# Performance work log

Hardware: AMD Instinct MI355X
Metric: run time of the kernel (lower is better)

Reference implementation:

```python
import jax, jax.numpy as jnp
import numpy as np

BN_EPS = 1e-5


def setup_inputs() -> dict:
    key = jax.random.key(0)
    ks = jax.random.split(key, 8)
    B, S, D, H, O = 4, 25000, 128, 128, 128
    N, E = B * S, 600000
    x = jax.random.normal(ks[0], (B, S, D), dtype=jnp.float32)
    edge_index = jax.random.randint(ks[1], (2, E), 0, N)
    W1 = jax.random.normal(ks[2], (D, H), dtype=jnp.float32) * (1.0 / np.sqrt(D))
    b1 = jnp.zeros((H,), jnp.float32)
    gamma1 = jnp.ones((H,), jnp.float32)
    beta1 = jnp.zeros((H,), jnp.float32)
    W2 = jax.random.normal(ks[3], (H, O), dtype=jnp.float32) * (1.0 / np.sqrt(H))
    b2 = jnp.zeros((O,), jnp.float32)
    return {"x": x, "edge_index": edge_index, "W1": W1, "b1": b1,
            "gamma1": gamma1, "beta1": beta1, "W2": W2, "b2": b2}


def _gcn_norm(edge_index, num_nodes, dtype):
    # PyG gcn_norm: add self-loops, symmetric D^-1/2 (A+I) D^-1/2 edge weights.
    row, col = edge_index
    loop = jnp.arange(num_nodes, dtype=row.dtype)
    row_f = jnp.concatenate([row, loop])
    col_f = jnp.concatenate([col, loop])
    deg = jax.ops.segment_sum(jnp.ones(row_f.shape, dtype), row_f,
                              num_segments=num_nodes)
    dis = jnp.where(deg > 0, jax.lax.rsqrt(jnp.maximum(deg, 1e-12)), 0.0)
    norm = dis[row_f] * dis[col_f]  # [E + N]
    return row_f, col_f, norm


def _gcn_conv(h, W, b, row_f, col_f, norm, num_nodes):
    hw = h @ W                       # [N, out]
    msg = hw[col_f] * norm[:, None]  # gather + scale, [E+N, out]
    out = jax.ops.segment_sum(msg, row_f, num_segments=num_nodes)
    return out + b


def reference(x, edge_index, W1, b1, gamma1, beta1, W2, b2):
    B, S, D = x.shape
    N = B * S
    h = x.reshape(N, D)
    row_f, col_f, norm = _gcn_norm(edge_index, N, h.dtype)
    # layer 1: GCNConv -> BatchNorm (batch stats) -> ReLU (dropout inactive in eval)
    h = _gcn_conv(h, W1, b1, row_f, col_f, norm, N)
    mean = jnp.mean(h, axis=0)
    var = jnp.mean(jnp.square(h - mean), axis=0)
    h = gamma1 * (h - mean) * jax.lax.rsqrt(var + BN_EPS) + beta1
    h = jax.nn.relu(h)
    # layer 2: final GCNConv
    h = _gcn_conv(h, W2, b2, row_f, col_f, norm, N)
    return h.reshape(B, S, -1)
```

## Files before the change

### kernel.cpp

```cpp
#include <hip/hip_runtime.h>

#define DIM 128
#define BN_EPS 1e-5f
#define STAT_COPIES 64

typedef short short8 __attribute__((ext_vector_type(8)));
typedef float floatx4 __attribute__((ext_vector_type(4)));

__device__ __forceinline__ unsigned short f2bf(float f) {
    unsigned int u = __builtin_bit_cast(unsigned int, f);
    u += 0x7FFFu + ((u >> 16) & 1u);
    return (unsigned short)(u >> 16);
}
__device__ __forceinline__ float bf2f(unsigned short h) {
    return __builtin_bit_cast(float, (unsigned int)h << 16);
}


__global__ __launch_bounds__(256) void deg_convw_kernel(
    const int* __restrict__ row, int* __restrict__ deg, int* __restrict__ rank,
    int E, int degB,
    const float* __restrict__ W1, const float* __restrict__ W2,
    unsigned short* __restrict__ wfrag)
{
    if ((int)blockIdx.x < degB) {
        int e = blockIdx.x * 256 + threadIdx.x;
        if (e < E) rank[e] = atomicAdd(&deg[row[e]], 1);
    } else {
        int s = (blockIdx.x - degB) * 256 + threadIdx.x;
        if (s >= 4096) return;
        int m  = s >> 11;
        int s2 = s & 2047;
        int kt = s2 >> 9;
        int nt = (s2 >> 6) & 7;
        int l  = s2 & 63;
        const float* W = m ? W2 : W1;
        unsigned short* o = wfrag + (size_t)m * 16384 + (size_t)s2 * 8;
        int k0 = kt * 32 + (l >> 4) * 8;
        int n0 = nt * 16 + (l & 15);
        #pragma unroll
        for (int j = 0; j < 8; ++j) o[j] = f2bf(W[(k0 + j) * DIM + n0]);
    }
}


__global__ __launch_bounds__(256) void scan_block_kernel(const int* __restrict__ deg,
                                                         int* __restrict__ rowptr,
                                                         int* __restrict__ aux,
                                                         float* __restrict__ dis, int n) {
    __shared__ int ls[256];
    const int base = blockIdx.x * 1024;
    const int t = threadIdx.x;
    int v[4]; int s = 0;
    #pragma unroll
    for (int k = 0; k < 4; ++k) {
        int i = base + t * 4 + k;
        v[k] = (i < n) ? deg[i] : 0;
        s += v[k];
    }
    ls[t] = s;
    __syncthreads();
    for (int off = 1; off < 256; off <<= 1) {
        int x = (t >= off) ? ls[t - off] : 0;
        __syncthreads();
        ls[t] += x;
        __syncthreads();
    }
    int excl = ls[t] - s;
    if (t == 255) aux[blockIdx.x] = ls[255];
    #pragma unroll
    for (int k = 0; k < 4; ++k) {
        int i = base + t * 4 + k;
        if (i < n) {
            rowptr[i] = excl;
            dis[i] = rsqrtf((float)(v[k] + 1));
        }
        excl += v[k];
    }
}


__global__ __launch_bounds__(256) void add_offsets_kernel(
    const int* __restrict__ rowptr, const int* __restrict__ deg,
    const int* __restrict__ aux, int2* __restrict__ rp2, int n)
{
    __shared__ int red[256];
    const int t = threadIdx.x;
    red[t] = (t < (int)blockIdx.x) ? aux[t] : 0;
    __syncthreads();
    for (int off = 128; off > 0; off >>= 1) {
        if (t < off) red[t] += red[t + off];
        __syncthreads();
    }
    const int base = red[0];
    #pragma unroll
    for (int k = 0; k < 4; ++k) {
        int i = blockIdx.x * 1024 + t * 4 + k;
        if (i < n) {
            int st = rowptr[i] + base;
            rp2[i] = make_int2(st, st + deg[i]);
        }
    }
}


__global__ __launch_bounds__(256) void scatter_gemm1_kernel(
    const int* __restrict__ row, const int* __restrict__ col,
    const int* __restrict__ rank, const float* __restrict__ dis,
    const int2* __restrict__ rp2, int2* __restrict__ epack, int E, int scatS,
    const float* __restrict__ A, const unsigned short* __restrict__ wfrag,
    unsigned short* __restrict__ C, int n, int gemmG)
{
    const int grp = blockIdx.x / 5;
    const int off = blockIdx.x % 5;
    if (off < 3) {
        const int sId = grp * 3 + off;
        if (sId >= scatS) return;
        int e = sId * 256 + threadIdx.x;
        if (e >= E) return;
        int r = row[e], c = col[e];
        int pos = rp2[r].x + rank[e];
        float nrm = dis[r] * dis[c];
        epack[pos] = make_int2(c, __builtin_bit_cast(int, nrm));
    } else {
        const int gId = grp * 2 + (off - 3);
        if (gId >= gemmG) return;
        const int tid  = threadIdx.x;
        const int row0 = gId * 64;
        const int wave = tid >> 6;
        const int lane = tid & 63;
        const int m    = lane & 15;
        const int quad = lane >> 4;
        const int rowA = row0 + wave * 16 + m;

        short8 af[4];
        if (rowA < n) {
            #pragma unroll
            for (int kt = 0; kt < 4; ++kt) {
                const float* src = A + (size_t)rowA * DIM + kt * 32 + quad * 8;
                float4 v0 = *(const float4*)(src);
                float4 v1 = *(const float4*)(src + 4);
                af[kt] = (short8){ (short)f2bf(v0.x), (short)f2bf(v0.y),
                                   (short)f2bf(v0.z), (short)f2bf(v0.w),
                                   (short)f2bf(v1.x), (short)f2bf(v1.y),
                                   (short)f2bf(v1.z), (short)f2bf(v1.w) };
            }
        } else {
            #pragma unroll
            for (int kt = 0; kt < 4; ++kt) af[kt] = (short8){0,0,0,0,0,0,0,0};
        }

        floatx4 acc[8];
        #pragma unroll
        for (int nt = 0; nt < 8; ++nt) acc[nt] = (floatx4){0.f, 0.f, 0.f, 0.f};

        #pragma unroll
        for (int nt = 0; nt < 8; ++nt)
            #pragma unroll
            for (int kt = 0; kt < 4; ++kt) {
                short8 bfr = *(const short8*)(wfrag + ((size_t)(kt * 8 + nt) * 64 + lane) * 8);
                acc[nt] = __builtin_amdgcn_mfma_f32_16x16x32_bf16(af[kt], bfr, acc[nt], 0, 0, 0);
            }

        #pragma unroll
        for (int nt = 0; nt < 8; ++nt)
            #pragma unroll
            for (int r = 0; r < 4; ++r) {
                int rr = row0 + wave * 16 + quad * 4 + r;
                if (rr < n) C[(size_t)rr * DIM + nt * 16 + m] = f2bf(acc[nt][r]);
            }
    }
}


__global__ __launch_bounds__(256) void gemm_mfma_bn_kernel(
    const unsigned short* __restrict__ Abf, const unsigned short* __restrict__ wfrag,
    unsigned short* __restrict__ C, int n,
    const float* __restrict__ mi)
{
    const int tid  = threadIdx.x;
    const int row0 = blockIdx.x * 64;
    const int wave = tid >> 6;
    const int lane = tid & 63;
    const int m    = lane & 15;
    const int quad = lane >> 4;
    const int rowA = row0 + wave * 16 + m;

    short8 af[4];
    if (rowA < n) {
        #pragma unroll
        for (int kt = 0; kt < 4; ++kt) {
            const int c0 = kt * 32 + quad * 8;
            short8 v = *(const short8*)(Abf + (size_t)rowA * DIM + c0);
            float4 s0 = *(const float4*)(mi + c0);
            float4 s1 = *(const float4*)(mi + c0 + 4);
            float4 h0 = *(const float4*)(mi + 128 + c0);
            float4 h1 = *(const float4*)(mi + 128 + c0 + 4);
            float f[8];
            #pragma unroll
            for (int j = 0; j < 8; ++j) f[j] = bf2f((unsigned short)v[j]);
            f[0] = fmaxf(fmaf(f[0], s0.x, h0.x), 0.f);
            f[1] = fmaxf(fmaf(f[1], s0.y, h0.y), 0.f);
            f[2] = fmaxf(fmaf(f[2], s0.z, h0.z), 0.f);
            f[3] = fmaxf(fmaf(f[3], s0.w, h0.w), 0.f);
            f[4] = fmaxf(fmaf(f[4], s1.x, h1.x), 0.f);
            f[5] = fmaxf(fmaf(f[5], s1.y, h1.y), 0.f);
            f[6] = fmaxf(fmaf(f[6], s1.z, h1.z), 0.f);
            f[7] = fmaxf(fmaf(f[7], s1.w, h1.w), 0.f);
            af[kt] = (short8){ (short)f2bf(f[0]), (short)f2bf(f[1]),
                               (short)f2bf(f[2]), (short)f2bf(f[3]),
                               (short)f2bf(f[4]), (short)f2bf(f[5]),
                               (short)f2bf(f[6]), (short)f2bf(f[7]) };
        }
    } else {
        #pragma unroll
        for (int kt = 0; kt < 4; ++kt) af[kt] = (short8){0,0,0,0,0,0,0,0};
    }

    floatx4 acc[8];
    #pragma unroll
    for (int nt = 0; nt < 8; ++nt) acc[nt] = (floatx4){0.f, 0.f, 0.f, 0.f};

    #pragma unroll
    for (int nt = 0; nt < 8; ++nt)
        #pragma unroll
        for (int kt = 0; kt < 4; ++kt) {
            short8 bfr = *(const short8*)(wfrag + ((size_t)(kt * 8 + nt) * 64 + lane) * 8);
            acc[nt] = __builtin_amdgcn_mfma_f32_16x16x32_bf16(af[kt], bfr, acc[nt], 0, 0, 0);
        }

    #pragma unroll
    for (int nt = 0; nt < 8; ++nt)
        #pragma unroll
        for (int r = 0; r < 4; ++r) {
            int rr = row0 + wave * 16 + quad * 4 + r;
            if (rr < n) C[(size_t)rr * DIM + nt * 16 + m] = f2bf(acc[nt][r]);
        }
}


__device__ __forceinline__ void acc8(float* acc, uint4 u, float w) {
    unsigned int a[4] = {u.x, u.y, u.z, u.w};
    #pragma unroll
    for (int k = 0; k < 4; ++k) {
        acc[2*k]   = fmaf(bf2f((unsigned short)(a[k] & 0xffff)), w, acc[2*k]);
        acc[2*k+1] = fmaf(bf2f((unsigned short)(a[k] >> 16)),    w, acc[2*k+1]);
    }
}

template <bool OUT_BF16, bool STATS>
__global__ __launch_bounds__(256) void agg_csr_kernel(
    const unsigned short* __restrict__ hw, const float* __restrict__ dis,
    const int2* __restrict__ rp2, const int2* __restrict__ epack,
    const float* __restrict__ bias, void* __restrict__ out_, int n,
    float* __restrict__ stat)
{
    const int sub  = threadIdx.x >> 4;
    const int l    = threadIdx.x & 15;
    const int node = blockIdx.x * 16 + sub;
    const bool valid = node < n;
    const int j = l * 8;

    float acc[8];
    #pragma unroll
    for (int k = 0; k < 8; ++k) acc[k] = 0.f;

    if (valid) {
        const int2 rp = rp2[node];
        {
            const float d = dis[node];
            uint4 u = *(const uint4*)(hw + (size_t)node * DIM + j);
            acc8(acc, u, d * d);
        }

        const int pe = rp.y;
        for (int p = rp.x; p < pe; p += 8) {
            const int pm = pe - 1;
            int2 e[8];
            #pragma unroll
            for (int k = 0; k < 8; ++k) {
                int pk = p + k;
                e[k] = epack[pk < pm ? pk : pm];
            }
            uint4 u[8];
            #pragma unroll
            for (int k = 0; k < 8; ++k)
                u[k] = *(const uint4*)(hw + (size_t)e[k].x * DIM + j);
            #pragma unroll
            for (int k = 0; k < 8; ++k) {
                float w = (p + k < pe) ? __builtin_bit_cast(float, e[k].y) : 0.f;
                acc8(acc, u[k], w);
            }
        }

        float4 b0 = *(const float4*)(bias + j);
        float4 b1 = *(const float4*)(bias + j + 4);
        acc[0] += b0.x; acc[1] += b0.y; acc[2] += b0.z; acc[3] += b0.w;
        acc[4] += b1.x; acc[5] += b1.y; acc[6] += b1.z; acc[7] += b1.w;

        if (OUT_BF16) {
            unsigned short* out = (unsigned short*)out_;
            uint4 o;
            o.x = (unsigned int)f2bf(acc[0]) | ((unsigned int)f2bf(acc[1]) << 16);
            o.y = (unsigned int)f2bf(acc[2]) | ((unsigned int)f2bf(acc[3]) << 16);
            o.z = (unsigned int)f2bf(acc[4]) | ((unsigned int)f2bf(acc[5]) << 16);
            o.w = (unsigned int)f2bf(acc[6]) | ((unsigned int)f2bf(acc[7]) << 16);
            *(uint4*)(out + (size_t)node * DIM + j) = o;
        } else {
            float* out = (float*)out_;
            *(float4*)(out + (size_t)node * DIM + j)     = make_float4(acc[0], acc[1], acc[2], acc[3]);
            *(float4*)(out + (size_t)node * DIM + j + 4) = make_float4(acc[4], acc[5], acc[6], acc[7]);
        }
    }

    if constexpr (STATS) {
        __shared__ float red[16][257];
        #pragma unroll
        for (int k = 0; k < 8; ++k) {
            float a = valid ? acc[k] : 0.f;
            red[sub][j + k]       = a;
            red[sub][128 + j + k] = a * a;
        }
        __syncthreads();
        float t = 0.f;
        #pragma unroll
        for (int r = 0; r < 16; ++r) t += red[r][threadIdx.x];
        atomicAdd(&stat[(blockIdx.x & (STAT_COPIES - 1)) * 256 + threadIdx.x], t);
    }
}


__global__ void bn_finalize_kernel(const float* __restrict__ stat,
                                   const float* __restrict__ gamma,
                                   const float* __restrict__ beta,
                                   float* __restrict__ mi, int n) {
    int c = threadIdx.x;
    if (c < DIM) {
        float s = 0.f, q = 0.f;
        #pragma unroll 4
        for (int cp = 0; cp < STAT_COPIES; ++cp) {
            s += stat[cp * 256 + c];
            q += stat[cp * 256 + 128 + c];
        }
        float mean  = s / (float)n;
        float var   = q / (float)n - mean * mean;
        float istd  = rsqrtf(var + BN_EPS);
        float scale = gamma[c] * istd;
        mi[c]       = scale;
        mi[DIM + c] = fmaf(-mean, scale, beta[c]);
    }
}


extern "C" void kernel_launch(void* const* d_in, const int* in_sizes, int n_in,
                              void* d_out, int out_size, void* d_ws, size_t ws_size,
                              hipStream_t stream)
{
    const float* x      = (const float*)d_in[0];
    const int*   ei     = (const int*)  d_in[1];
    const float* W1     = (const float*)d_in[2];
    const float* b1     = (const float*)d_in[3];
    const float* gamma1 = (const float*)d_in[4];
    const float* beta1  = (const float*)d_in[5];
    const float* W2     = (const float*)d_in[6];
    const float* b2     = (const float*)d_in[7];
    float* out = (float*)d_out;

    const int N = in_sizes[0] / DIM;
    const int E = in_sizes[1] / 2;
    const int* row = ei;
    const int* col = ei + E;

    const int NB    = (N + 1023) / 1024;
    const int degB  = (E + 255) / 256;
    const int gemmB = (N + 63) / 64;
    const int aggB  = (N + 15) / 16;
    const int k4B   = 5 * max((degB + 2) / 3, (gemmB + 1) / 2);

    unsigned short* hw    = (unsigned short*)d_ws;
    unsigned short* h1    = hw + (size_t)N * DIM;
    int2*  epack  = (int2*)(h1 + (size_t)N * DIM);
    int2*  rp2    = epack + E;
    unsigned short* wfrag = (unsigned short*)(rp2 + N);
    float* dis    = (float*)(wfrag + 2 * 16384);
    int*   rank   = (int*)(dis + N);
    int*   rowptr = rank + E;
    int*   aux    = rowptr + N;
    float* mi     = (float*)(aux + 256);
    int*   deg    = (int*)(mi + 256);
    float* stat   = (float*)(deg + N);
    const size_t zero_bytes = (size_t)N * 4 + (size_t)STAT_COPIES * 256 * 4;

    hipMemsetAsync(deg, 0, zero_bytes, stream);

    deg_convw_kernel<<<degB + 16, 256, 0, stream>>>(row, deg, rank, E, degB, W1, W2, wfrag);
    scan_block_kernel<<<NB, 256, 0, stream>>>(deg, rowptr, aux, dis, N);
    add_offsets_kernel<<<NB, 256, 0, stream>>>(rowptr, deg, aux, rp2, N);
    scatter_gemm1_kernel<<<k4B, 256, 0, stream>>>(row, col, rank, dis, rp2, epack, E, degB,
                                                  x, wfrag, hw, N, gemmB);
    agg_csr_kernel<true, true><<<aggB, 256, 0, stream>>>(hw, dis, rp2, epack, b1, h1, N,
                                                         stat);
    bn_finalize_kernel<<<1, DIM, 0, stream>>>(stat, gamma1, beta1, mi, N);
    gemm_mfma_bn_kernel<<<gemmB, 256, 0, stream>>>(h1, wfrag + 16384, hw, N, mi);
    agg_csr_kernel<false, false><<<aggB, 256, 0, stream>>>(hw, dis, rp2, epack, b2, out, N,
                                                           nullptr);
}
```

Before: 261.9 us.

## Reorder layer-2 as aggregate-then-transform and fuse BN/ReLU, aggregation and GEMM

Layer 2 now aggregates the normalized, ReLU'd h1 features first and multiplies by W2 afterwards (A·(h·W) = (A·h)·W). The BN and ReLU are applied on the fly to every gathered neighbor row, and a per-block fp32 FMA GEMM against W2 runs in the same kernel. This removes the separate MFMA GEMM kernel and its bf16 intermediate write and re-read. In exchange BN/ReLU is recomputed once per edge, and the W2 product runs on scalar FMAs reading W2 from global memory instead of using MFMA.

```diff
diff --git a/kernel.cpp b/kernel.cpp
--- a/kernel.cpp
+++ b/kernel.cpp
@@ -20,26 +20,22 @@
 __global__ __launch_bounds__(256) void deg_convw_kernel(
     const int* __restrict__ row, int* __restrict__ deg, int* __restrict__ rank,
     int E, int degB,
-    const float* __restrict__ W1, const float* __restrict__ W2,
-    unsigned short* __restrict__ wfrag)
+    const float* __restrict__ W1, unsigned short* __restrict__ wfrag)
 {
     if ((int)blockIdx.x < degB) {
         int e = blockIdx.x * 256 + threadIdx.x;
         if (e < E) rank[e] = atomicAdd(&deg[row[e]], 1);
     } else {
         int s = (blockIdx.x - degB) * 256 + threadIdx.x;
-        if (s >= 4096) return;
-        int m  = s >> 11;
-        int s2 = s & 2047;
-        int kt = s2 >> 9;
-        int nt = (s2 >> 6) & 7;
-        int l  = s2 & 63;
-        const float* W = m ? W2 : W1;
-        unsigned short* o = wfrag + (size_t)m * 16384 + (size_t)s2 * 8;
+        if (s >= 2048) return;
+        int kt = s >> 9;
+        int nt = (s >> 6) & 7;
+        int l  = s & 63;
+        unsigned short* o = wfrag + (size_t)s * 8;
         int k0 = kt * 32 + (l >> 4) * 8;
         int n0 = nt * 16 + (l & 15);
         #pragma unroll
-        for (int j = 0; j < 8; ++j) o[j] = f2bf(W[(k0 + j) * DIM + n0]);
+        for (int j = 0; j < 8; ++j) o[j] = f2bf(W1[(k0 + j) * DIM + n0]);
     }
 }
 
@@ -173,72 +169,6 @@
 }
 
 
-__global__ __launch_bounds__(256) void gemm_mfma_bn_kernel(
-    const unsigned short* __restrict__ Abf, const unsigned short* __restrict__ wfrag,
-    unsigned short* __restrict__ C, int n,
-    const float* __restrict__ mi)
-{
-    const int tid  = threadIdx.x;
-    const int row0 = blockIdx.x * 64;
-    const int wave = tid >> 6;
-    const int lane = tid & 63;
-    const int m    = lane & 15;
-    const int quad = lane >> 4;
-    const int rowA = row0 + wave * 16 + m;
-
-    short8 af[4];
-    if (rowA < n) {
-        #pragma unroll
-        for (int kt = 0; kt < 4; ++kt) {
-            const int c0 = kt * 32 + quad * 8;
-            short8 v = *(const short8*)(Abf + (size_t)rowA * DIM + c0);
-            float4 s0 = *(const float4*)(mi + c0);
-            float4 s1 = *(const float4*)(mi + c0 + 4);
-            float4 h0 = *(const float4*)(mi + 128 + c0);
-            float4 h1 = *(const float4*)(mi + 128 + c0 + 4);
-            float f[8];
-            #pragma unroll
-            for (int j = 0; j < 8; ++j) f[j] = bf2f((unsigned short)v[j]);
-            f[0] = fmaxf(fmaf(f[0], s0.x, h0.x), 0.f);
-            f[1] = fmaxf(fmaf(f[1], s0.y, h0.y), 0.f);
-            f[2] = fmaxf(fmaf(f[2], s0.z, h0.z), 0.f);
-            f[3] = fmaxf(fmaf(f[3], s0.w, h0.w), 0.f);
-            f[4] = fmaxf(fmaf(f[4], s1.x, h1.x), 0.f);
-            f[5] = fmaxf(fmaf(f[5], s1.y, h1.y), 0.f);
-            f[6] = fmaxf(fmaf(f[6], s1.z, h1.z), 0.f);
-            f[7] = fmaxf(fmaf(f[7], s1.w, h1.w), 0.f);
-            af[kt] = (short8){ (short)f2bf(f[0]), (short)f2bf(f[1]),
-                               (short)f2bf(f[2]), (short)f2bf(f[3]),
-                               (short)f2bf(f[4]), (short)f2bf(f[5]),
-                               (short)f2bf(f[6]), (short)f2bf(f[7]) };
-        }
-    } else {
-        #pragma unroll
-        for (int kt = 0; kt < 4; ++kt) af[kt] = (short8){0,0,0,0,0,0,0,0};
-    }
-
-    floatx4 acc[8];
-    #pragma unroll
-    for (int nt = 0; nt < 8; ++nt) acc[nt] = (floatx4){0.f, 0.f, 0.f, 0.f};
-
-    #pragma unroll
-    for (int nt = 0; nt < 8; ++nt)
-        #pragma unroll
-        for (int kt = 0; kt < 4; ++kt) {
-            short8 bfr = *(const short8*)(wfrag + ((size_t)(kt * 8 + nt) * 64 + lane) * 8);
-            acc[nt] = __builtin_amdgcn_mfma_f32_16x16x32_bf16(af[kt], bfr, acc[nt], 0, 0, 0);
-        }
-
-    #pragma unroll
-    for (int nt = 0; nt < 8; ++nt)
-        #pragma unroll
-        for (int r = 0; r < 4; ++r) {
-            int rr = row0 + wave * 16 + quad * 4 + r;
-            if (rr < n) C[(size_t)rr * DIM + nt * 16 + m] = f2bf(acc[nt][r]);
-        }
-}
-
-
 __device__ __forceinline__ void acc8(float* acc, uint4 u, float w) {
     unsigned int a[4] = {u.x, u.y, u.z, u.w};
     #pragma unroll
@@ -248,11 +178,10 @@
     }
 }
 
-template <bool OUT_BF16, bool STATS>
-__global__ __launch_bounds__(256) void agg_csr_kernel(
+__global__ __launch_bounds__(256) void agg1_kernel(
     const unsigned short* __restrict__ hw, const float* __restrict__ dis,
     const int2* __restrict__ rp2, const int2* __restrict__ epack,
-    const float* __restrict__ bias, void* __restrict__ out_, int n,
+    const float* __restrict__ bias, unsigned short* __restrict__ out, int n,
     float* __restrict__ stat)
 {
     const int sub  = threadIdx.x >> 4;
@@ -298,35 +227,26 @@
         acc[0] += b0.x; acc[1] += b0.y; acc[2] += b0.z; acc[3] += b0.w;
         acc[4] += b1.x; acc[5] += b1.y; acc[6] += b1.z; acc[7] += b1.w;
 
-        if (OUT_BF16) {
-            unsigned short* out = (unsigned short*)out_;
-            uint4 o;
-            o.x = (unsigned int)f2bf(acc[0]) | ((unsigned int)f2bf(acc[1]) << 16);
-            o.y = (unsigned int)f2bf(acc[2]) | ((unsigned int)f2bf(acc[3]) << 16);
-            o.z = (unsigned int)f2bf(acc[4]) | ((unsigned int)f2bf(acc[5]) << 16);
-            o.w = (unsigned int)f2bf(acc[6]) | ((unsigned int)f2bf(acc[7]) << 16);
-            *(uint4*)(out + (size_t)node * DIM + j) = o;
-        } else {
-            float* out = (float*)out_;
-            *(float4*)(out + (size_t)node * DIM + j)     = make_float4(acc[0], acc[1], acc[2], acc[3]);
-            *(float4*)(out + (size_t)node * DIM + j + 4) = make_float4(acc[4], acc[5], acc[6], acc[7]);
-        }
-    }
-
-    if constexpr (STATS) {
-        __shared__ float red[16][257];
-        #pragma unroll
-        for (int k = 0; k < 8; ++k) {
-            float a = valid ? acc[k] : 0.f;
-            red[sub][j + k]       = a;
-            red[sub][128 + j + k] = a * a;
-        }
-        __syncthreads();
-        float t = 0.f;
-        #pragma unroll
-        for (int r = 0; r < 16; ++r) t += red[r][threadIdx.x];
-        atomicAdd(&stat[(blockIdx.x & (STAT_COPIES - 1)) * 256 + threadIdx.x], t);
-    }
+        uint4 o;
+        o.x = (unsigned int)f2bf(acc[0]) | ((unsigned int)f2bf(acc[1]) << 16);
+        o.y = (unsigned int)f2bf(acc[2]) | ((unsigned int)f2bf(acc[3]) << 16);
+        o.z = (unsigned int)f2bf(acc[4]) | ((unsigned int)f2bf(acc[5]) << 16);
+        o.w = (unsigned int)f2bf(acc[6]) | ((unsigned int)f2bf(acc[7]) << 16);
+        *(uint4*)(out + (size_t)node * DIM + j) = o;
+    }
+
+    __shared__ float red[16][257];
+    #pragma unroll
+    for (int k = 0; k < 8; ++k) {
+        float a = valid ? acc[k] : 0.f;
+        red[sub][j + k]       = a;
+        red[sub][128 + j + k] = a * a;
+    }
+    __syncthreads();
+    float t = 0.f;
+    #pragma unroll
+    for (int r = 0; r < 16; ++r) t += red[r][threadIdx.x];
+    atomicAdd(&stat[(blockIdx.x & (STAT_COPIES - 1)) * 256 + threadIdx.x], t);
 }
 
 
@@ -348,6 +268,104 @@
         float scale = gamma[c] * istd;
         mi[c]       = scale;
         mi[DIM + c] = fmaf(-mean, scale, beta[c]);
+    }
+}
+
+
+__global__ __launch_bounds__(256) void agg2_gemm_kernel(
+    const unsigned short* __restrict__ h1, const float* __restrict__ dis,
+    const int2* __restrict__ rp2, const int2* __restrict__ epack,
+    const float* __restrict__ W2,
+    const float* __restrict__ mi,
+    const float* __restrict__ b2,
+    float* __restrict__ out, int n)
+{
+    __shared__ float sSf[16][132];
+    const int tid  = threadIdx.x;
+    const int sub  = tid >> 4;
+    const int l    = tid & 15;
+    const int node0 = blockIdx.x * 16;
+    const int node = node0 + sub;
+    const bool valid = node < n;
+    const int j = l * 8;
+
+    float sc[8], sh[8];
+    #pragma unroll
+    for (int k = 0; k < 8; ++k) { sc[k] = mi[j + k]; sh[k] = mi[128 + j + k]; }
+
+    float acc[8];
+    #pragma unroll
+    for (int k = 0; k < 8; ++k) acc[k] = 0.f;
+
+    if (valid) {
+        const int2 rp = rp2[node];
+        {
+            const float d = dis[node];
+            const float dd = d * d;
+            uint4 u = *(const uint4*)(h1 + (size_t)node * DIM + j);
+            unsigned int a[4] = {u.x, u.y, u.z, u.w};
+            #pragma unroll
+            for (int k = 0; k < 4; ++k) {
+                float z0 = fmaxf(fmaf(bf2f((unsigned short)(a[k] & 0xffff)), sc[2*k],   sh[2*k]),   0.f);
+                float z1 = fmaxf(fmaf(bf2f((unsigned short)(a[k] >> 16)),    sc[2*k+1], sh[2*k+1]), 0.f);
+                acc[2*k]   = fmaf(z0, dd, acc[2*k]);
+                acc[2*k+1] = fmaf(z1, dd, acc[2*k+1]);
+            }
+        }
+
+        const int pe = rp.y;
+        for (int p = rp.x; p < pe; p += 8) {
+            const int pm = pe - 1;
+            int2 e[8];
+            #pragma unroll
+            for (int k = 0; k < 8; ++k) {
+                int pk = p + k;
+                e[k] = epack[pk < pm ? pk : pm];
+            }
+            uint4 u[8];
+            #pragma unroll
+            for (int k = 0; k < 8; ++k)
+                u[k] = *(const uint4*)(h1 + (size_t)e[k].x * DIM + j);
+            #pragma unroll
+            for (int k = 0; k < 8; ++k) {
+                float w = (p + k < pe) ? __builtin_bit_cast(float, e[k].y) : 0.f;
+                unsigned int a[4] = {u[k].x, u[k].y, u[k].z, u[k].w};
+                #pragma unroll
+                for (int q = 0; q < 4; ++q) {
+                    float z0 = fmaxf(fmaf(bf2f((unsigned short)(a[q] & 0xffff)), sc[2*q],   sh[2*q]),   0.f);
+                    float z1 = fmaxf(fmaf(bf2f((unsigned short)(a[q] >> 16)),    sc[2*q+1], sh[2*q+1]), 0.f);
+                    acc[2*q]   = fmaf(z0, w, acc[2*q]);
+                    acc[2*q+1] = fmaf(z1, w, acc[2*q+1]);
+                }
+            }
+        }
+    }
+
+    *(float4*)(&sSf[sub][j])     = make_float4(acc[0], acc[1], acc[2], acc[3]);
+    *(float4*)(&sSf[sub][j + 4]) = make_float4(acc[4], acc[5], acc[6], acc[7]);
+    __syncthreads();
+
+    float4 bb0 = *(const float4*)(b2 + j);
+    float4 bb1 = *(const float4*)(b2 + j + 4);
+    float o[8] = { bb0.x, bb0.y, bb0.z, bb0.w, bb1.x, bb1.y, bb1.z, bb1.w };
+    #pragma unroll 4
+    for (int k = 0; k < DIM; ++k) {
+        float sv = sSf[sub][k];
+        float4 w0 = *(const float4*)(W2 + (size_t)k * DIM + j);
+        float4 w1 = *(const float4*)(W2 + (size_t)k * DIM + j + 4);
+        o[0] = fmaf(sv, w0.x, o[0]);
+        o[1] = fmaf(sv, w0.y, o[1]);
+        o[2] = fmaf(sv, w0.z, o[2]);
+        o[3] = fmaf(sv, w0.w, o[3]);
+        o[4] = fmaf(sv, w1.x, o[4]);
+        o[5] = fmaf(sv, w1.y, o[5]);
+        o[6] = fmaf(sv, w1.z, o[6]);
+        o[7] = fmaf(sv, w1.w, o[7]);
+    }
+
+    if (valid) {
+        *(float4*)(out + (size_t)node * DIM + j)     = make_float4(o[0], o[1], o[2], o[3]);
+        *(float4*)(out + (size_t)node * DIM + j + 4) = make_float4(o[4], o[5], o[6], o[7]);
     }
 }
 
@@ -393,15 +411,12 @@
 
     hipMemsetAsync(deg, 0, zero_bytes, stream);
 
-    deg_convw_kernel<<<degB + 16, 256, 0, stream>>>(row, deg, rank, E, degB, W1, W2, wfrag);
+    deg_convw_kernel<<<degB + 8, 256, 0, stream>>>(row, deg, rank, E, degB, W1, wfrag);
     scan_block_kernel<<<NB, 256, 0, stream>>>(deg, rowptr, aux, dis, N);
     add_offsets_kernel<<<NB, 256, 0, stream>>>(rowptr, deg, aux, rp2, N);
     scatter_gemm1_kernel<<<k4B, 256, 0, stream>>>(row, col, rank, dis, rp2, epack, E, degB,
                                                   x, wfrag, hw, N, gemmB);
-    agg_csr_kernel<true, true><<<aggB, 256, 0, stream>>>(hw, dis, rp2, epack, b1, h1, N,
-                                                         stat);
+    agg1_kernel<<<aggB, 256, 0, stream>>>(hw, dis, rp2, epack, b1, h1, N, stat);
     bn_finalize_kernel<<<1, DIM, 0, stream>>>(stat, gamma1, beta1, mi, N);
-    gemm_mfma_bn_kernel<<<gemmB, 256, 0, stream>>>(h1, wfrag + 16384, hw, N, mi);
-    agg_csr_kernel<false, false><<<aggB, 256, 0, stream>>>(hw, dis, rp2, epack, b2, out, N,
-                                                           nullptr);
-}
+    agg2_gemm_kernel<<<aggB, 256, 0, stream>>>(h1, dis, rp2, epack, W2, mi, b2, out, N);
+}
```

Result: slower. 412.6 us (+57.5%).
